# Performance work log

Hardware: AMD Instinct MI355X
Metric: run time of the kernel (lower is better)

The kernel has to match this reference:

```python
import jax, jax.numpy as jnp
import numpy as np

# Production-scale dims (see shape_source)
B, N_C, N_T = 2, 4096, 1024
D_X, D_S = 64, 3
K = 32                 # SGNP default k=32
RECALL = 0.95          # approx_min_k recall_target as in approx_knn
SX = SS = ST = 1.0     # scale_x_sim / scale_s_sim / scale_t_sim


def setup_inputs() -> dict:
    key = jax.random.key(0)
    ks = jax.random.split(key, 6)
    return {
        "x_ctx": jax.random.normal(ks[0], (B, N_C, D_X), jnp.float32),
        "s_ctx": jax.random.normal(ks[1], (B, N_C, D_S), jnp.float32),
        "t_ctx": jax.random.uniform(ks[2], (B, N_C, 1), dtype=jnp.float32),
        "mask_ctx": jnp.ones((B, N_C), dtype=bool),
        "x_test": jax.random.normal(ks[3], (B, N_T, D_X), jnp.float32),
        "s_test": jax.random.normal(ks[4], (B, N_T, D_S), jnp.float32),
        "t_test": jax.random.uniform(ks[5], (B, N_T, 1), dtype=jnp.float32),
    }


def _sq_cdist(q, r):
    # squared euclidean distance, [B,Nq,d] x [B,Nr,d] -> [B,Nq,Nr]
    qn = jnp.sum(q * q, axis=-1)
    rn = jnp.sum(r * r, axis=-1)
    return qn[:, :, None] + rn[:, None, :] - 2.0 * jnp.einsum("bqd,brd->bqr", q, r)


def _knn(qx, qs, qt, rx, rs, rt, mask):
    """Vectorized approx_knn: multi-modal distances, causal mask, top-k, gather."""
    inf = jnp.inf
    m = mask[:, None, :]                       # [B,1,Nr] -> masked refs get inf (as _safe_mask)
    d_x = jnp.where(m, _sq_cdist(qx, rx), inf)  # [B,Nq,Nr]
    d_s = jnp.where(m, _sq_cdist(qs, rs), inf)
    d_t = rt[:, None, :, 0] - qt[:, :, None, 0]  # signed time diff (r - q)
    d_t = jnp.where(m, d_t, inf)
    d_t = jnp.where(d_t <= 0, d_t, inf)          # causal_t mask
    d_sq = (SX * d_x) ** 2 + (SS * d_s) ** 2 + (ST * d_t) ** 2
    _, idx = jax.lax.approx_min_k(jax.lax.stop_gradient(d_sq), K, recall_target=RECALL)
    g = lambda d: jnp.take_along_axis(d, idx, axis=-1)  # [B,Nq,K]
    return idx, g(d_x), g(d_s), g(d_t)


def reference(x_ctx, s_ctx, t_ctx, mask_ctx, x_test, s_test, t_test):
    # ctx->ctx and test->ctx kNN (build_graph)
    idx_cc, dx_cc, ds_cc, dt_cc = _knn(x_ctx, s_ctx, t_ctx, x_ctx, s_ctx, t_ctx, mask_ctx)
    idx_ct, dx_ct, ds_ct, dt_ct = _knn(x_test, s_test, t_test, x_ctx, s_ctx, t_ctx, mask_ctx)

    # batch offsets into the flat node array [B*N_C ctx nodes, then B*N_T test nodes]
    off = jnp.arange(B) * N_C
    senders_cc = idx_cc.reshape(-1) + jnp.repeat(off, N_C * K)
    senders_ct = idx_ct.reshape(-1) + jnp.repeat(off, N_T * K)
    senders = jnp.concatenate([senders_cc, senders_ct])
    receivers = jnp.repeat(jnp.arange(B * (N_C + N_T)), K)

    cat = lambda a, b: jnp.concatenate([a.reshape(-1), b.reshape(-1)])
    d_x = cat(dx_cc, dx_ct)   # [B*(N_C+N_T)*K]
    d_s = cat(ds_cc, ds_ct)
    d_t = cat(dt_cc, dt_ct)
    edge_mask = jnp.isfinite(d_x) & jnp.isfinite(d_s) & jnp.isfinite(d_t)
    return senders, receivers, d_x, d_s, d_t, edge_mask
```

## Files before the change

kernel.cpp:

```cpp
#include <hip/hip_runtime.h>

namespace {
constexpr int kB  = 2;
constexpr int kNC = 4096;
constexpr int kNT = 1024;
constexpr int kDX = 64;
constexpr int kK  = 32;
constexpr int kNQ = kB * (kNC + kNT);
constexpr long long kE = (long long)kNQ * kK;
constexpr int QPW  = 4;
constexpr int WAVES = 4;
constexpr int QPB  = WAVES * QPW;
constexpr int TILE = 64;
constexpr int NT   = kNC / TILE;
constexpr float kBigFinite = 1e30f;
}

__device__ __forceinline__ void resolve_q(int gid,
    const float* x_ctx, const float* s_ctx, const float* t_ctx,
    const float* x_test, const float* s_test, const float* t_test,
    int& b, const float*& qx, const float*& qs, const float*& qt)
{
    if (gid < kB * kNC) {
        b  = gid >> 12;
        qx = x_ctx + (size_t)gid * kDX;
        qs = s_ctx + (size_t)gid * 3;
        qt = t_ctx + gid;
    } else {
        const int g2 = gid - kB * kNC;
        b  = g2 >> 10;
        qx = x_test + (size_t)g2 * kDX;
        qs = s_test + (size_t)g2 * 3;
        qt = t_test + g2;
    }
}

__device__ __forceinline__ void insert_half(unsigned long long& listKey,
    unsigned long long keyQ, int lane, int base)
{
    const unsigned long long thr = __shfl(listKey, base + 31, 64);
    unsigned long long hb = __ballot(keyQ < thr);
    while (hb) {
        const int srcl = __ffsll((unsigned long long)hb) - 1;
        hb &= hb - 1;
        const unsigned long long K = __shfl(keyQ, srcl, 64);
        const unsigned long long lt = __ballot(listKey < K);
        const unsigned int half = base ? (unsigned int)(lt >> 32)
                                       : (unsigned int)lt;
        const int pos = __popc(half) + base;
        if (pos < base + 32) {
            const unsigned long long up = __shfl_up(listKey, 1, 64);
            if (lane >= base && lane < base + 32) {
                if (lane > pos)       listKey = up;
                else if (lane == pos) listKey = K;
            }
        }
    }
}

__global__ __launch_bounds__(256, 4)
void knn_v4(const float* __restrict__ x_ctx, const float* __restrict__ s_ctx,
            const float* __restrict__ t_ctx, const unsigned char* __restrict__ mask_ctx,
            const float* __restrict__ x_test, const float* __restrict__ s_test,
            const float* __restrict__ t_test, float* __restrict__ out)
{
    __shared__ float4 xt[2][TILE * 16];

    const int tid  = threadIdx.x;
    const int lane = tid & 63;
    const int w    = __builtin_amdgcn_readfirstlane(tid >> 6);
    const int qbase = blockIdx.x * QPB;
    const int gid0  = qbase + w * QPW;

    int b;
    { int b_; const float *a, *c, *d;
      resolve_q(qbase, x_ctx, s_ctx, t_ctx, x_test, s_test, t_test, b_, a, c, d);
      b = b_; }

    const float4* xb4 = (const float4*)x_ctx + (size_t)b * kNC * (kDX / 4);
    const float*  rsp = s_ctx + (size_t)b * kNC * 3;
    const float*  rtp = t_ctx + (size_t)b * kNC;
    const unsigned char* mp = mask_ctx + (size_t)b * kNC;

    const float* qxp[QPW];
    float qs0[QPW], qs1[QPW], qs2[QPW], qsn[QPW], qtv[QPW], qn[QPW];
    #pragma unroll
    for (int q = 0; q < QPW; ++q) {
        int bb; const float *qx, *qs, *qt;
        resolve_q(gid0 + q, x_ctx, s_ctx, t_ctx, x_test, s_test, t_test,
                  bb, qx, qs, qt);
        qxp[q] = qx;
        qs0[q] = qs[0]; qs1[q] = qs[1]; qs2[q] = qs[2]; qtv[q] = qt[0];
        qsn[q] = qs0[q]*qs0[q] + qs1[q]*qs1[q] + qs2[q]*qs2[q];
        const float ql = qx[lane];
        float s = ql * ql;
        #pragma unroll
        for (int off = 32; off > 0; off >>= 1) s += __shfl_xor(s, off, 64);
        qn[q] = s;
    }

    int sg[4], ss[4];
    #pragma unroll
    for (int i = 0; i < 4; ++i) {
        const int n = tid + 256 * i;
        const int r = n >> 4, j = n & 15;
        sg[i] = n;
        ss[i] = (r << 4) | (j ^ (r & 7));
    }
    #pragma unroll
    for (int i = 0; i < 4; ++i) xt[0][ss[i]] = xb4[sg[i]];
    __syncthreads();

    const int lbase = lane << 4, lsw = lane & 7;
    const float INF = __builtin_inff();
    unsigned long long lst01 = ~0ull, lst23 = ~0ull;

    for (int t = 0; t < NT; ++t) {
        float4 p0, p1, p2, p3;
        const bool pre = (t + 1 < NT);
        if (pre) {
            const size_t nb = (size_t)(t + 1) * 1024;
            p0 = xb4[nb + sg[0]]; p1 = xb4[nb + sg[1]];
            p2 = xb4[nb + sg[2]]; p3 = xb4[nb + sg[3]];
        }
        const float4* buf = xt[t & 1];

        float dot[QPW] = {0.f, 0.f, 0.f, 0.f};
        float rn = 0.f;
        #pragma unroll
        for (int j = 0; j < 16; ++j) {
            const float4 rv = buf[lbase | (j ^ lsw)];
            rn = fmaf(rv.x, rv.x, rn); rn = fmaf(rv.y, rv.y, rn);
            rn = fmaf(rv.z, rv.z, rn); rn = fmaf(rv.w, rv.w, rn);
            #pragma unroll
            for (int q = 0; q < QPW; ++q) {
                const float4 qv = ((const float4*)qxp[q])[j];
                dot[q] = fmaf(qv.x, rv.x, dot[q]);
                dot[q] = fmaf(qv.y, rv.y, dot[q]);
                dot[q] = fmaf(qv.z, rv.z, dot[q]);
                dot[q] = fmaf(qv.w, rv.w, dot[q]);
            }
        }

        const int r = t * TILE + lane;
        const float rs0 = rsp[r*3+0], rs1 = rsp[r*3+1], rs2 = rsp[r*3+2];
        const float rtv = rtp[r];
        const bool  m   = (mp[r] != 0);
        const float rsn = rs0*rs0 + rs1*rs1 + rs2*rs2;

        #pragma unroll
        for (int q = 0; q < QPW; ++q) {
            float d_x = qn[q] + rn - 2.0f * dot[q];
            const float sdot = qs0[q]*rs0 + qs1[q]*rs1 + qs2[q]*rs2;
            float d_s = qsn[q] + rsn - 2.0f * sdot;
            float d_t = rtv - qtv[q];
            if (!m) { d_x = INF; d_s = INF; d_t = INF; }
            if (!(d_t <= 0.f)) d_t = INF;
            const float v = d_x*d_x + d_s*d_s + d_t*d_t;
            const unsigned long long key =
                ((unsigned long long)__float_as_uint(v) << 32) | (unsigned)r;
            if (q < 2) insert_half(lst01, key, lane, (q & 1) * 32);
            else       insert_half(lst23, key, lane, (q & 1) * 32);
        }

        if (pre) {
            float4* nbuf = xt[(t + 1) & 1];
            nbuf[ss[0]] = p0; nbuf[ss[1]] = p1;
            nbuf[ss[2]] = p2; nbuf[ss[3]] = p3;
        }
        __syncthreads();
    }

    #pragma unroll
    for (int p = 0; p < 2; ++p) {
        const unsigned long long myl = p ? lst23 : lst01;
        const int qidx = 2 * p + (lane >> 5);
        const int rsel = (int)(myl & 0xFFFFFFFFull);
        const int gid  = gid0 + qidx;
        const float* qx  = (lane < 32) ? qxp[2*p] : qxp[2*p+1];
        const float qn_  = (lane < 32) ? qn [2*p] : qn [2*p+1];
        const float qs0_ = (lane < 32) ? qs0[2*p] : qs0[2*p+1];
        const float qs1_ = (lane < 32) ? qs1[2*p] : qs1[2*p+1];
        const float qs2_ = (lane < 32) ? qs2[2*p] : qs2[2*p+1];
        const float qsn_ = (lane < 32) ? qsn[2*p] : qsn[2*p+1];
        const float qtv_ = (lane < 32) ? qtv[2*p] : qtv[2*p+1];

        const float4* xr = (const float4*)(x_ctx + ((size_t)b * kNC + rsel) * kDX);
        const float4* qr = (const float4*)qx;
        float dot = 0.f, rn2 = 0.f;
        #pragma unroll
        for (int j = 0; j < 16; ++j) {
            const float4 rv = xr[j];
            const float4 qv = qr[j];
            rn2 = fmaf(rv.x, rv.x, rn2); rn2 = fmaf(rv.y, rv.y, rn2);
            rn2 = fmaf(rv.z, rv.z, rn2); rn2 = fmaf(rv.w, rv.w, rn2);
            dot = fmaf(qv.x, rv.x, dot); dot = fmaf(qv.y, rv.y, dot);
            dot = fmaf(qv.z, rv.z, dot); dot = fmaf(qv.w, rv.w, dot);
        }
        float d_x = qn_ + rn2 - 2.0f * dot;
        const float rs0 = rsp[rsel*3+0], rs1 = rsp[rsel*3+1], rs2 = rsp[rsel*3+2];
        const float rsn = rs0*rs0 + rs1*rs1 + rs2*rs2;
        const float sdot = qs0_*rs0 + qs1_*rs1 + qs2_*rs2;
        float d_s = qsn_ + rsn - 2.0f * sdot;
        const float dt_raw = rtp[rsel] - qtv_;
        const bool  m = (mp[rsel] != 0);
        const bool  causal = m && (dt_raw <= 0.f);

        const float em = causal ? 1.0f : 0.0f;
        const float d_x_out = m ? d_x : kBigFinite;
        const float d_s_out = m ? d_s : kBigFinite;
        const float d_t_out = causal ? dt_raw : kBigFinite;

        const size_t e = (size_t)gid * kK + (size_t)(lane & 31);
        out[e]                = (float)(rsel + b * kNC);
        out[(size_t)kE   + e] = (float)gid;
        out[(size_t)kE*2 + e] = d_x_out;
        out[(size_t)kE*3 + e] = d_s_out;
        out[(size_t)kE*4 + e] = d_t_out;
        out[(size_t)kE*5 + e] = em;
    }
}

extern "C" void kernel_launch(void* const* d_in, const int* in_sizes, int n_in,
                              void* d_out, int out_size, void* d_ws, size_t ws_size,
                              hipStream_t stream) {
    (void)in_sizes; (void)n_in; (void)d_ws; (void)ws_size; (void)out_size;
    const float* x_ctx = (const float*)d_in[0];
    const float* s_ctx = (const float*)d_in[1];
    const float* t_ctx = (const float*)d_in[2];
    const unsigned char* mask_ctx = (const unsigned char*)d_in[3];
    const float* x_test = (const float*)d_in[4];
    const float* s_test = (const float*)d_in[5];
    const float* t_test = (const float*)d_in[6];

    knn_v4<<<dim3(kNQ / QPB), dim3(256), 0, stream>>>(
        x_ctx, s_ctx, t_ctx, mask_ctx, x_test, s_test, t_test, (float*)d_out);
}
```

Before: 372.3 us.

## Split kNN reference scan into two halves with a merge kernel and precomputed norms

Adds a three-kernel path. A prep kernel precomputes reference squared norms. The partial kNN kernel scans only half of the context per block, doubling the block count so more blocks can be in flight, and writes per-half top-32 keys to workspace. A merge kernel combines the two sorted lists by rank counting and recomputes the output distances. The aim is more parallelism and less per-tile norm arithmetic, at the cost of two extra launches and workspace traffic. The old single-kernel path is kept as a fallback when the workspace is too small.

```diff
diff --git a/kernel.cpp b/kernel.cpp
--- a/kernel.cpp
+++ b/kernel.cpp
@@ -12,8 +12,12 @@
 constexpr int WAVES = 4;
 constexpr int QPB  = WAVES * QPW;
 constexpr int TILE = 64;
-constexpr int NT   = kNC / TILE;
+constexpr int HALF = 2048;
+constexpr int HT   = HALF / TILE;
 constexpr float kBigFinite = 1e30f;
+constexpr size_t kRNF     = 8192;
+constexpr size_t kKeyOffB = kRNF * 4;
+constexpr size_t kWsNeed  = kKeyOffB + (size_t)kNQ * 64 * 8;
 }
 
 __device__ __forceinline__ void resolve_q(int gid,
@@ -58,18 +62,37 @@
     }
 }
 
-__global__ __launch_bounds__(256, 4)
-void knn_v4(const float* __restrict__ x_ctx, const float* __restrict__ s_ctx,
-            const float* __restrict__ t_ctx, const unsigned char* __restrict__ mask_ctx,
-            const float* __restrict__ x_test, const float* __restrict__ s_test,
-            const float* __restrict__ t_test, float* __restrict__ out)
+__global__ __launch_bounds__(256)
+void prep_rn(const float* __restrict__ x, float* __restrict__ ws)
+{
+    const int r = blockIdx.x * 256 + threadIdx.x;
+    const float4* xr = (const float4*)(x + (size_t)r * kDX);
+    float rn = 0.f;
+    #pragma unroll
+    for (int j = 0; j < 16; ++j) {
+        const float4 rv = xr[j];
+        rn = fmaf(rv.x, rv.x, rn); rn = fmaf(rv.y, rv.y, rn);
+        rn = fmaf(rv.z, rv.z, rn); rn = fmaf(rv.w, rv.w, rn);
+    }
+    ws[r] = rn;
+}
+
+__global__ __launch_bounds__(256, 5)
+void knn_v5_part(const float* __restrict__ x_ctx, const float* __restrict__ s_ctx,
+                 const float* __restrict__ t_ctx, const unsigned char* __restrict__ mask_ctx,
+                 const float* __restrict__ x_test, const float* __restrict__ s_test,
+                 const float* __restrict__ t_test, const float* __restrict__ rn_ws,
+                 unsigned long long* __restrict__ keys)
 {
     __shared__ float4 xt[2][TILE * 16];
 
     const int tid  = threadIdx.x;
     const int lane = tid & 63;
     const int w    = __builtin_amdgcn_readfirstlane(tid >> 6);
-    const int qbase = blockIdx.x * QPB;
+    const int blk  = blockIdx.x;
+    const int g    = blk >> 1;
+    const int h    = blk & 1;
+    const int qbase = g * QPB;
     const int gid0  = qbase + w * QPW;
 
     int b;
@@ -80,6 +103,7 @@
     const float4* xb4 = (const float4*)x_ctx + (size_t)b * kNC * (kDX / 4);
     const float*  rsp = s_ctx + (size_t)b * kNC * 3;
     const float*  rtp = t_ctx + (size_t)b * kNC;
+    const float*  rnp = rn_ws + (size_t)b * kNC;
     const unsigned char* mp = mask_ctx + (size_t)b * kNC;
 
     const float* qxp[QPW];
@@ -107,24 +131,215 @@
         sg[i] = n;
         ss[i] = (r << 4) | (j ^ (r & 7));
     }
-    #pragma unroll
-    for (int i = 0; i < 4; ++i) xt[0][ss[i]] = xb4[sg[i]];
+    const size_t hbase = (size_t)h * (HALF * 16);
+    #pragma unroll
+    for (int i = 0; i < 4; ++i) xt[0][ss[i]] = xb4[hbase + sg[i]];
     __syncthreads();
 
     const int lbase = lane << 4, lsw = lane & 7;
     const float INF = __builtin_inff();
     unsigned long long lst01 = ~0ull, lst23 = ~0ull;
 
-    for (int t = 0; t < NT; ++t) {
+    for (int t = 0; t < HT; ++t) {
         float4 p0, p1, p2, p3;
-        const bool pre = (t + 1 < NT);
+        const bool pre = (t + 1 < HT);
+        if (pre) {
+            const size_t nb = hbase + (size_t)(t + 1) * 1024;
+            p0 = xb4[nb + sg[0]]; p1 = xb4[nb + sg[1]];
+            p2 = xb4[nb + sg[2]]; p3 = xb4[nb + sg[3]];
+        }
+        const float4* buf = xt[t & 1];
+
+        float dot[QPW] = {0.f, 0.f, 0.f, 0.f};
+        #pragma unroll
+        for (int j = 0; j < 16; ++j) {
+            const float4 rv = buf[lbase | (j ^ lsw)];
+            #pragma unroll
+            for (int q = 0; q < QPW; ++q) {
+                const float4 qv = ((const float4*)qxp[q])[j];
+                dot[q] = fmaf(qv.x, rv.x, dot[q]);
+                dot[q] = fmaf(qv.y, rv.y, dot[q]);
+                dot[q] = fmaf(qv.z, rv.z, dot[q]);
+                dot[q] = fmaf(qv.w, rv.w, dot[q]);
+            }
+        }
+
+        const int r = h * HALF + t * TILE + lane;
+        const float rn  = rnp[r];
+        const float rs0 = rsp[r*3+0], rs1 = rsp[r*3+1], rs2 = rsp[r*3+2];
+        const float rtv = rtp[r];
+        const bool  m   = (mp[r] != 0);
+        const float rsn = rs0*rs0 + rs1*rs1 + rs2*rs2;
+
+        #pragma unroll
+        for (int q = 0; q < QPW; ++q) {
+            float d_x = qn[q] + rn - 2.0f * dot[q];
+            const float sdot = qs0[q]*rs0 + qs1[q]*rs1 + qs2[q]*rs2;
+            float d_s = qsn[q] + rsn - 2.0f * sdot;
+            float d_t = rtv - qtv[q];
+            if (!m) { d_x = INF; d_s = INF; d_t = INF; }
+            if (!(d_t <= 0.f)) d_t = INF;
+            const float v = d_x*d_x + d_s*d_s + d_t*d_t;
+            const unsigned long long key =
+                ((unsigned long long)__float_as_uint(v) << 32) | (unsigned)r;
+            if (q < 2) insert_half(lst01, key, lane, (q & 1) * 32);
+            else       insert_half(lst23, key, lane, (q & 1) * 32);
+        }
+
+        if (pre) {
+            float4* nbuf = xt[(t + 1) & 1];
+            nbuf[ss[0]] = p0; nbuf[ss[1]] = p1;
+            nbuf[ss[2]] = p2; nbuf[ss[3]] = p3;
+        }
+        __syncthreads();
+    }
+
+    #pragma unroll
+    for (int p = 0; p < 2; ++p) {
+        const unsigned long long key = p ? lst23 : lst01;
+        const int qidx = 2 * p + (lane >> 5);
+        keys[((size_t)(gid0 + qidx) * 2 + h) * 32 + (lane & 31)] = key;
+    }
+}
+
+__global__ __launch_bounds__(256)
+void knn_v5_merge(const float* __restrict__ x_ctx, const float* __restrict__ s_ctx,
+                  const float* __restrict__ t_ctx, const unsigned char* __restrict__ mask_ctx,
+                  const float* __restrict__ x_test, const float* __restrict__ s_test,
+                  const float* __restrict__ t_test,
+                  const unsigned long long* __restrict__ keys,
+                  float* __restrict__ out)
+{
+    __shared__ unsigned long long kbuf[WAVES][64];
+    __shared__ unsigned long long merged[WAVES][32];
+
+    const int tid  = threadIdx.x;
+    const int lane = tid & 63;
+    const int w    = tid >> 6;
+    const int qid  = blockIdx.x * WAVES + w;
+
+    int b; const float *qx, *qs, *qt;
+    resolve_q(qid, x_ctx, s_ctx, t_ctx, x_test, s_test, t_test, b, qx, qs, qt);
+    const float qs0_ = qs[0], qs1_ = qs[1], qs2_ = qs[2], qtv_ = qt[0];
+    const float qsn_ = qs0_*qs0_ + qs1_*qs1_ + qs2_*qs2_;
+    const float ql = qx[lane];
+    float qn_ = ql * ql;
+    #pragma unroll
+    for (int off = 32; off > 0; off >>= 1) qn_ += __shfl_xor(qn_, off, 64);
+
+    const unsigned long long mykey = keys[(size_t)qid * 64 + lane];
+    kbuf[w][lane] = mykey;
+    __syncthreads();
+
+    int cnt = 0;
+    const int ob = (lane < 32) ? 32 : 0;
+    #pragma unroll
+    for (int j = 0; j < 32; ++j) cnt += (kbuf[w][ob + j] < mykey) ? 1 : 0;
+    const int pos = (lane & 31) + cnt;
+    if (pos < 32) merged[w][pos] = mykey;
+    __syncthreads();
+
+    if (lane < kK) {
+        const unsigned long long key = merged[w][lane];
+        const int rsel = (int)(key & 0xFFFFFFFFull);
+
+        const float*  rsp = s_ctx + (size_t)b * kNC * 3;
+        const float*  rtp = t_ctx + (size_t)b * kNC;
+        const unsigned char* mp = mask_ctx + (size_t)b * kNC;
+
+        const float4* xr = (const float4*)(x_ctx + ((size_t)b * kNC + rsel) * kDX);
+        const float4* qr = (const float4*)qx;
+        float dot = 0.f, rn2 = 0.f;
+        #pragma unroll
+        for (int j = 0; j < 16; ++j) {
+            const float4 rv = xr[j];
+            const float4 qv = qr[j];
+            rn2 = fmaf(rv.x, rv.x, rn2); rn2 = fmaf(rv.y, rv.y, rn2);
+            rn2 = fmaf(rv.z, rv.z, rn2); rn2 = fmaf(rv.w, rv.w, rn2);
+            dot = fmaf(qv.x, rv.x, dot); dot = fmaf(qv.y, rv.y, dot);
+            dot = fmaf(qv.z, rv.z, dot); dot = fmaf(qv.w, rv.w, dot);
+        }
+        float d_x = qn_ + rn2 - 2.0f * dot;
+        const float rs0 = rsp[rsel*3+0], rs1 = rsp[rsel*3+1], rs2 = rsp[rsel*3+2];
+        const float rsn = rs0*rs0 + rs1*rs1 + rs2*rs2;
+        const float sdot = qs0_*rs0 + qs1_*rs1 + qs2_*rs2;
+        float d_s = qsn_ + rsn - 2.0f * sdot;
+        const float dt_raw = rtp[rsel] - qtv_;
+        const bool  m = (mp[rsel] != 0);
+        const bool  causal = m && (dt_raw <= 0.f);
+
+        const float em = causal ? 1.0f : 0.0f;
+        const float d_x_out = m ? d_x : kBigFinite;
+        const float d_s_out = m ? d_s : kBigFinite;
+        const float d_t_out = causal ? dt_raw : kBigFinite;
+
+        const size_t e = (size_t)qid * kK + (size_t)lane;
+        out[e]                = (float)(rsel + b * kNC);
+        out[(size_t)kE   + e] = (float)qid;
+        out[(size_t)kE*2 + e] = d_x_out;
+        out[(size_t)kE*3 + e] = d_s_out;
+        out[(size_t)kE*4 + e] = d_t_out;
+        out[(size_t)kE*5 + e] = em;
+    }
+}
+
+__global__ __launch_bounds__(256, 4)
+void knn_v4(const float* __restrict__ x_ctx, const float* __restrict__ s_ctx,
+            const float* __restrict__ t_ctx, const unsigned char* __restrict__ mask_ctx,
+            const float* __restrict__ x_test, const float* __restrict__ s_test,
+            const float* __restrict__ t_test, float* __restrict__ out)
+{
+    __shared__ float4 xt[2][TILE * 16];
+    const int tid  = threadIdx.x;
+    const int lane = tid & 63;
+    const int w    = __builtin_amdgcn_readfirstlane(tid >> 6);
+    const int qbase = blockIdx.x * QPB;
+    const int gid0  = qbase + w * QPW;
+    int b;
+    { int b_; const float *a, *c, *d;
+      resolve_q(qbase, x_ctx, s_ctx, t_ctx, x_test, s_test, t_test, b_, a, c, d);
+      b = b_; }
+    const float4* xb4 = (const float4*)x_ctx + (size_t)b * kNC * (kDX / 4);
+    const float*  rsp = s_ctx + (size_t)b * kNC * 3;
+    const float*  rtp = t_ctx + (size_t)b * kNC;
+    const unsigned char* mp = mask_ctx + (size_t)b * kNC;
+    const float* qxp[QPW];
+    float qs0[QPW], qs1[QPW], qs2[QPW], qsn[QPW], qtv[QPW], qn[QPW];
+    #pragma unroll
+    for (int q = 0; q < QPW; ++q) {
+        int bb; const float *qx, *qs, *qt;
+        resolve_q(gid0 + q, x_ctx, s_ctx, t_ctx, x_test, s_test, t_test, bb, qx, qs, qt);
+        qxp[q] = qx;
+        qs0[q] = qs[0]; qs1[q] = qs[1]; qs2[q] = qs[2]; qtv[q] = qt[0];
+        qsn[q] = qs0[q]*qs0[q] + qs1[q]*qs1[q] + qs2[q]*qs2[q];
+        const float ql = qx[lane];
+        float s = ql * ql;
+        #pragma unroll
+        for (int off = 32; off > 0; off >>= 1) s += __shfl_xor(s, off, 64);
+        qn[q] = s;
+    }
+    int sg[4], ss[4];
+    #pragma unroll
+    for (int i = 0; i < 4; ++i) {
+        const int n = tid + 256 * i;
+        const int r = n >> 4, j = n & 15;
+        sg[i] = n; ss[i] = (r << 4) | (j ^ (r & 7));
+    }
+    #pragma unroll
+    for (int i = 0; i < 4; ++i) xt[0][ss[i]] = xb4[sg[i]];
+    __syncthreads();
+    const int lbase = lane << 4, lsw = lane & 7;
+    const float INF = __builtin_inff();
+    unsigned long long lst01 = ~0ull, lst23 = ~0ull;
+    for (int t = 0; t < kNC / TILE; ++t) {
+        float4 p0, p1, p2, p3;
+        const bool pre = (t + 1 < kNC / TILE);
         if (pre) {
             const size_t nb = (size_t)(t + 1) * 1024;
             p0 = xb4[nb + sg[0]]; p1 = xb4[nb + sg[1]];
             p2 = xb4[nb + sg[2]]; p3 = xb4[nb + sg[3]];
         }
         const float4* buf = xt[t & 1];
-
         float dot[QPW] = {0.f, 0.f, 0.f, 0.f};
         float rn = 0.f;
         #pragma unroll
@@ -141,13 +356,11 @@
                 dot[q] = fmaf(qv.w, rv.w, dot[q]);
             }
         }
-
         const int r = t * TILE + lane;
         const float rs0 = rsp[r*3+0], rs1 = rsp[r*3+1], rs2 = rsp[r*3+2];
         const float rtv = rtp[r];
         const bool  m   = (mp[r] != 0);
         const float rsn = rs0*rs0 + rs1*rs1 + rs2*rs2;
-
         #pragma unroll
         for (int q = 0; q < QPW; ++q) {
             float d_x = qn[q] + rn - 2.0f * dot[q];
@@ -162,7 +375,6 @@
             if (q < 2) insert_half(lst01, key, lane, (q & 1) * 32);
             else       insert_half(lst23, key, lane, (q & 1) * 32);
         }
-
         if (pre) {
             float4* nbuf = xt[(t + 1) & 1];
             nbuf[ss[0]] = p0; nbuf[ss[1]] = p1;
@@ -170,7 +382,6 @@
         }
         __syncthreads();
     }
-
     #pragma unroll
     for (int p = 0; p < 2; ++p) {
         const unsigned long long myl = p ? lst23 : lst01;
@@ -184,7 +395,6 @@
         const float qs2_ = (lane < 32) ? qs2[2*p] : qs2[2*p+1];
         const float qsn_ = (lane < 32) ? qsn[2*p] : qsn[2*p+1];
         const float qtv_ = (lane < 32) ? qtv[2*p] : qtv[2*p+1];
-
         const float4* xr = (const float4*)(x_ctx + ((size_t)b * kNC + rsel) * kDX);
         const float4* qr = (const float4*)qx;
         float dot = 0.f, rn2 = 0.f;
@@ -205,18 +415,13 @@
         const float dt_raw = rtp[rsel] - qtv_;
         const bool  m = (mp[rsel] != 0);
         const bool  causal = m && (dt_raw <= 0.f);
-
         const float em = causal ? 1.0f : 0.0f;
-        const float d_x_out = m ? d_x : kBigFinite;
-        const float d_s_out = m ? d_s : kBigFinite;
-        const float d_t_out = causal ? dt_raw : kBigFinite;
-
         const size_t e = (size_t)gid * kK + (size_t)(lane & 31);
         out[e]                = (float)(rsel + b * kNC);
         out[(size_t)kE   + e] = (float)gid;
-        out[(size_t)kE*2 + e] = d_x_out;
-        out[(size_t)kE*3 + e] = d_s_out;
-        out[(size_t)kE*4 + e] = d_t_out;
+        out[(size_t)kE*2 + e] = m ? d_x : kBigFinite;
+        out[(size_t)kE*3 + e] = m ? d_s : kBigFinite;
+        out[(size_t)kE*4 + e] = causal ? dt_raw : kBigFinite;
         out[(size_t)kE*5 + e] = em;
     }
 }
@@ -224,7 +429,7 @@
 extern "C" void kernel_launch(void* const* d_in, const int* in_sizes, int n_in,
                               void* d_out, int out_size, void* d_ws, size_t ws_size,
                               hipStream_t stream) {
-    (void)in_sizes; (void)n_in; (void)d_ws; (void)ws_size; (void)out_size;
+    (void)in_sizes; (void)n_in; (void)out_size;
     const float* x_ctx = (const float*)d_in[0];
     const float* s_ctx = (const float*)d_in[1];
     const float* t_ctx = (const float*)d_in[2];
@@ -233,6 +438,18 @@
     const float* s_test = (const float*)d_in[5];
     const float* t_test = (const float*)d_in[6];
 
-    knn_v4<<<dim3(kNQ / QPB), dim3(256), 0, stream>>>(
-        x_ctx, s_ctx, t_ctx, mask_ctx, x_test, s_test, t_test, (float*)d_out);
-}
+    if (ws_size >= kWsNeed) {
+        float* rn_ws = (float*)d_ws;
+        unsigned long long* keys =
+            (unsigned long long*)((char*)d_ws + kKeyOffB);
+        prep_rn<<<dim3(32), dim3(256), 0, stream>>>(x_ctx, rn_ws);
+        knn_v5_part<<<dim3(2 * kNQ / QPB), dim3(256), 0, stream>>>(
+            x_ctx, s_ctx, t_ctx, mask_ctx, x_test, s_test, t_test, rn_ws, keys);
+        knn_v5_merge<<<dim3(kNQ / WAVES), dim3(256), 0, stream>>>(
+            x_ctx, s_ctx, t_ctx, mask_ctx, x_test, s_test, t_test, keys,
+            (float*)d_out);
+    } else {
+        knn_v4<<<dim3(kNQ / QPB), dim3(256), 0, stream>>>(
+            x_ctx, s_ctx, t_ctx, mask_ctx, x_test, s_test, t_test, (float*)d_out);
+    }
+}
```

Result: slower. 508.9 us (+36.7%).
